# Performance work log

Hardware: AMD Instinct MI355X
Metric: run time of the kernel (lower is better)

The kernel has to match this reference:

```python
import jax, jax.numpy as jnp
import numpy as np

V, E, H, NL, B, T = 32000, 256, 256, 2, 32, 256


def setup_inputs() -> dict:
    key = jax.random.key(0)
    ks = jax.random.split(key, 20)
    s = 0.05
    d = {}
    d['x'] = jax.random.randint(ks[0], (B, T), 0, V)
    d['encoder_output'] = jax.random.normal(ks[1], (T + 1, B, 2 * H), jnp.float32)
    d['encoder_final_state'] = jax.random.normal(ks[2], (2 * NL, B, H), jnp.float32)
    d['embedding'] = jax.random.normal(ks[3], (V, E), jnp.float32) * s
    d['enc_proj_w'] = jax.random.normal(ks[4], (H, 2 * H), jnp.float32) * s
    d['enc_proj_b'] = jnp.zeros((H,), jnp.float32)
    d['attn_wq'] = jax.random.normal(ks[5], (H, H), jnp.float32) * s
    d['attn_wk'] = jax.random.normal(ks[6], (H, H), jnp.float32) * s
    d['attn_wv'] = jax.random.normal(ks[7], (H,), jnp.float32) * s
    d['gru_w_ih0'] = jax.random.normal(ks[8], (3 * H, E + H), jnp.float32) * s
    d['gru_w_hh0'] = jax.random.normal(ks[9], (3 * H, H), jnp.float32) * s
    d['gru_b_ih0'] = jnp.zeros((3 * H,), jnp.float32)
    d['gru_b_hh0'] = jnp.zeros((3 * H,), jnp.float32)
    d['gru_w_ih1'] = jax.random.normal(ks[10], (3 * H, H), jnp.float32) * s
    d['gru_w_hh1'] = jax.random.normal(ks[11], (3 * H, H), jnp.float32) * s
    d['gru_b_ih1'] = jnp.zeros((3 * H,), jnp.float32)
    d['gru_b_hh1'] = jnp.zeros((3 * H,), jnp.float32)
    d['dense_w'] = jax.random.normal(ks[12], (V, H), jnp.float32) * s
    d['dense_b'] = jnp.zeros((V,), jnp.float32)
    return d


def _gru_cell(xin, h, w_ih, w_hh, b_ih, b_hh):
    gi = xin @ w_ih.T + b_ih
    gh = h @ w_hh.T + b_hh
    i_r, i_z, i_n = jnp.split(gi, 3, axis=-1)
    h_r, h_z, h_n = jnp.split(gh, 3, axis=-1)
    r = jax.nn.sigmoid(i_r + h_r)
    z = jax.nn.sigmoid(i_z + h_z)
    n = jnp.tanh(i_n + r * h_n)
    return (1.0 - z) * n + z * h


def _forward(x, encoder_output, encoder_final_state, embedding, enc_proj_w, enc_proj_b,
             attn_wq, attn_wk, attn_wv,
             gru_w_ih0, gru_w_hh0, gru_b_ih0, gru_b_hh0,
             gru_w_ih1, gru_w_hh1, gru_b_ih1, gru_b_hh1,
             dense_w, dense_b):
    Bb, Tt = x.shape
    Hh = enc_proj_w.shape[0]
    L = 2 * Tt  # fixed KV buffer length (= max attention width)
    # project encoder output: (B, T+1, H)
    proj = jnp.einsum('sbd,hd->bsh', encoder_output, enc_proj_w) + enc_proj_b
    # sum forward/backward encoder final states -> (n_layers, B, H)
    h0 = encoder_final_state.reshape(NL, 2, Bb, Hh).sum(axis=1)
    emb = embedding[x].transpose(1, 0, 2)  # (T, B, E)
    # fixed-size KV buffer; slots [0, T+1) hold projected encoder output
    kv0 = jnp.zeros((Bb, L, Hh), proj.dtype).at[:, :Tt + 1, :].set(proj)
    kproj0 = jnp.einsum('blh,gh->blg', kv0, attn_wk)  # precomputed key projections

    def step(carry, inp):
        h, kv, kproj = carry
        emb_t, t = inp
        q = h[-1] @ attn_wq.T  # (B, H)
        scores = jnp.tanh(kproj + q[:, None, :]) @ attn_wv  # (B, L)
        valid = jnp.arange(L) < (Tt + 1 + t)
        attn = jax.nn.softmax(jnp.where(valid[None, :], scores, -1e9), axis=-1)
        attn = attn * valid[None, :].astype(attn.dtype)  # exact zeros at padding
        context = jnp.einsum('bl,blh->bh', attn, kv)
        xin = jnp.concatenate([context, emb_t], axis=-1)  # (B, H+E)
        h0n = _gru_cell(xin, h[0], gru_w_ih0, gru_w_hh0, gru_b_ih0, gru_b_hh0)
        h1n = _gru_cell(h0n, h[1], gru_w_ih1, gru_w_hh1, gru_b_ih1, gru_b_hh1)
        h_new = jnp.stack([h0n, h1n], axis=0)
        out = h1n  # top-layer output for this timestep
        pos = Tt + 1 + t
        kv = jax.lax.dynamic_update_slice_in_dim(kv, out[:, None, :], pos, axis=1)
        kproj = jax.lax.dynamic_update_slice_in_dim(kproj, (out @ attn_wk.T)[:, None, :], pos, axis=1)
        return (h_new, kv, kproj), (out, attn)

    (_, _, _), (outs, attns) = jax.lax.scan(step, (h0, kv0, kproj0), (emb, jnp.arange(Tt)))
    outs = outs.transpose(1, 0, 2)  # (B, T, H)
    logits = jnp.einsum('bth,vh->btv', outs, dense_w) + dense_b  # (B, T, V)
    attn_scores = attns.transpose(1, 0, 2)  # (B, T, 2T)
    return logits, attn_scores


def reference(x, encoder_output, encoder_final_state, embedding, enc_proj_w, enc_proj_b,
              attn_wq, attn_wk, attn_wv,
              gru_w_ih0, gru_w_hh0, gru_b_ih0, gru_b_hh0,
              gru_w_ih1, gru_w_hh1, gru_b_ih1, gru_b_hh1,
              dense_w, dense_b):
    return _forward(x, encoder_output, encoder_final_state, embedding, enc_proj_w, enc_proj_b,
                    attn_wq, attn_wk, attn_wv,
                    gru_w_ih0, gru_w_hh0, gru_b_ih0, gru_b_hh0,
                    gru_w_ih1, gru_w_hh1, gru_b_ih1, gru_b_hh1,
                    dense_w, dense_b)
```

## Files before the change

kernel.cpp:

```cpp
#include <hip/hip_runtime.h>
#include <hip/hip_bf16.h>
#include <hip/hip_fp16.h>

#define NB 32
#define NT 256
#define NH 256
#define NV 32000
#define NL2 512
#define NTP1 257
#define KPS 260

typedef unsigned int u32x4 __attribute__((ext_vector_type(4)));
typedef unsigned int u32x2 __attribute__((ext_vector_type(2)));
typedef short s16x8 __attribute__((ext_vector_type(8)));
typedef float f32x4 __attribute__((ext_vector_type(4)));
typedef float f32x2 __attribute__((ext_vector_type(2)));
typedef _Float16 half2v __attribute__((ext_vector_type(2)));

#define AGENT __HIP_MEMORY_SCOPE_AGENT
__device__ __forceinline__ float aload(const float* p) {
  return __hip_atomic_load((float*)p, __ATOMIC_RELAXED, AGENT);
}
__device__ __forceinline__ void astore(float* p, float v) {
  __hip_atomic_store(p, v, __ATOMIC_RELAXED, AGENT);
}
__device__ __forceinline__ unsigned int aloadu(const unsigned int* p) {
  return __hip_atomic_load((unsigned int*)p, __ATOMIC_RELAXED, AGENT);
}
__device__ __forceinline__ void astoreu(unsigned int* p, unsigned int v) {
  __hip_atomic_store(p, v, __ATOMIC_RELAXED, AGENT);
}

__device__ __forceinline__ float dot2f(half2v a, half2v b, float c) {
#if __has_builtin(__builtin_amdgcn_fdot2)
  return __builtin_amdgcn_fdot2(a, b, c, false);
#else
  return c + (float)a[0] * (float)b[0] + (float)a[1] * (float)b[1];
#endif
}
__device__ __forceinline__ half2v h2(unsigned int u) { return __builtin_bit_cast(half2v, u); }

__device__ __forceinline__ float dotf16(const _Float16* __restrict__ w,
                                        const _Float16* __restrict__ x, int n, float acc) {
#pragma unroll 8
  for (int k = 0; k < n; k += 16) {
    u32x4 a0 = *(const u32x4*)(w + k);
    u32x4 a1 = *(const u32x4*)(w + k + 8);
    u32x4 b0 = *(const u32x4*)(x + k);
    u32x4 b1 = *(const u32x4*)(x + k + 8);
    acc = dot2f(h2(a0.x), h2(b0.x), acc);
    acc = dot2f(h2(a0.y), h2(b0.y), acc);
    acc = dot2f(h2(a0.z), h2(b0.z), acc);
    acc = dot2f(h2(a0.w), h2(b0.w), acc);
    acc = dot2f(h2(a1.x), h2(b1.x), acc);
    acc = dot2f(h2(a1.y), h2(b1.y), acc);
    acc = dot2f(h2(a1.z), h2(b1.z), acc);
    acc = dot2f(h2(a1.w), h2(b1.w), acc);
  }
  return acc;
}

__device__ __forceinline__ float dot16h(const _Float16* __restrict__ w,
                                        const _Float16* __restrict__ x) {
  u32x4 a0 = *(const u32x4*)w;
  u32x4 a1 = *(const u32x4*)(w + 8);
  u32x4 b0 = *(const u32x4*)x;
  u32x4 b1 = *(const u32x4*)(x + 8);
  float acc = 0.f;
  acc = dot2f(h2(a0.x), h2(b0.x), acc);
  acc = dot2f(h2(a0.y), h2(b0.y), acc);
  acc = dot2f(h2(a0.z), h2(b0.z), acc);
  acc = dot2f(h2(a0.w), h2(b0.w), acc);
  acc = dot2f(h2(a1.x), h2(b1.x), acc);
  acc = dot2f(h2(a1.y), h2(b1.y), acc);
  acc = dot2f(h2(a1.z), h2(b1.z), acc);
  acc = dot2f(h2(a1.w), h2(b1.w), acc);
  return acc;
}

__device__ __forceinline__ float fast_tanh(float x) {
  x = fminf(15.f, fmaxf(-15.f, x));
  float e = __expf(2.f * x);
  return 1.f - __fdividef(2.f, e + 1.f);
}
__device__ __forceinline__ float fast_sigmoid(float x) {
  x = fminf(30.f, fmaxf(-30.f, x));
  float e = __expf(-x);
  return __fdividef(1.f, 1.f + e);
}
__device__ __forceinline__ unsigned short f2bf(float f) {
  unsigned int u = __builtin_bit_cast(unsigned int, f);
  return (unsigned short)((u + 0x7FFFu + ((u >> 16) & 1u)) >> 16);
}

__device__ __forceinline__ void batch_barrier(int* __restrict__ ctr, int target) {
  __syncthreads();
  if (threadIdx.x == 0) {
    __hip_atomic_fetch_add(ctr, 1, __ATOMIC_RELEASE, AGENT);
    while (__hip_atomic_load(ctr, __ATOMIC_RELAXED, AGENT) < target)
      __builtin_amdgcn_s_sleep(1);
    asm volatile("" ::: "memory");
  }
  __syncthreads();
}


__global__ void conv_f16_kernel(const float* __restrict__ s, _Float16* __restrict__ d, int n) {
  int i = blockIdx.x * 256 + threadIdx.x;
  if (i < n) d[i] = (_Float16)s[i];
}

__global__ void conv_bf16_kernel(const float* __restrict__ s, unsigned short* __restrict__ d, int n) {
  int i = blockIdx.x * 256 + threadIdx.x;
  if (i < n) d[i] = f2bf(s[i]);
}

__global__ void transpose_kernel(const float* __restrict__ w, float* __restrict__ wT) {
  int i = blockIdx.x * 256 + threadIdx.x;
  if (i < 256 * 512) { int h = i >> 9, dd = i & 511; wT[dd * 256 + h] = w[i]; }
}

__global__ __launch_bounds__(256) void proj_kernel(const float* __restrict__ enc,
                                                   const float* __restrict__ wT,
                                                   const float* __restrict__ pb,
                                                   _Float16* __restrict__ kvT) {
  int gid = blockIdx.x * 256 + threadIdx.x;
  int h4 = gid & 63;
  int bs = gid >> 6;
  if (bs >= NTP1 * NB) return;
  int s = bs >> 5, b = bs & 31;
  const float* er = enc + (size_t)bs * 512;
  float a0 = 0.f, a1 = 0.f, a2 = 0.f, a3 = 0.f;
  for (int d = 0; d < 512; d += 4) {
    f32x4 e4 = *(const f32x4*)(er + d);
    f32x4 w0 = *(const f32x4*)(wT + (size_t)(d + 0) * 256 + h4 * 4);
    f32x4 w1 = *(const f32x4*)(wT + (size_t)(d + 1) * 256 + h4 * 4);
    f32x4 w2 = *(const f32x4*)(wT + (size_t)(d + 2) * 256 + h4 * 4);
    f32x4 w3 = *(const f32x4*)(wT + (size_t)(d + 3) * 256 + h4 * 4);
    a0 = fmaf(e4.x, w0.x, a0); a1 = fmaf(e4.x, w0.y, a1); a2 = fmaf(e4.x, w0.z, a2); a3 = fmaf(e4.x, w0.w, a3);
    a0 = fmaf(e4.y, w1.x, a0); a1 = fmaf(e4.y, w1.y, a1); a2 = fmaf(e4.y, w1.z, a2); a3 = fmaf(e4.y, w1.w, a3);
    a0 = fmaf(e4.z, w2.x, a0); a1 = fmaf(e4.z, w2.y, a1); a2 = fmaf(e4.z, w2.z, a2); a3 = fmaf(e4.z, w2.w, a3);
    a0 = fmaf(e4.w, w3.x, a0); a1 = fmaf(e4.w, w3.y, a1); a2 = fmaf(e4.w, w3.z, a2); a3 = fmaf(e4.w, w3.w, a3);
  }
  int h = h4 * 4;
  a0 += pb[h + 0]; a1 += pb[h + 1]; a2 += pb[h + 2]; a3 += pb[h + 3];
  size_t base = ((size_t)b * NH) * NL2 + s;
  kvT[base + (size_t)(h + 0) * NL2] = (_Float16)a0;
  kvT[base + (size_t)(h + 1) * NL2] = (_Float16)a1;
  kvT[base + (size_t)(h + 2) * NL2] = (_Float16)a2;
  kvT[base + (size_t)(h + 3) * NL2] = (_Float16)a3;
}

__global__ __launch_bounds__(256) void kproj0_kernel(const _Float16* __restrict__ kvT,
                                                     const float* __restrict__ wk,
                                                     _Float16* __restrict__ kprojL) {
  int b = blockIdx.x >> 3, gq = blockIdx.x & 7;
  __shared__ float wks[32][256];
  __shared__ float pk[32][8];
  int tid = threadIdx.x;
  for (int i = tid; i < 32 * 256; i += 256) {
    int g = i >> 8, h = i & 255;
    wks[g][h] = wk[(size_t)(gq * 32 + g) * 256 + h];
  }
  __syncthreads();
  {
    int l = tid;
    float acc[32];
#pragma unroll
    for (int g = 0; g < 32; ++g) acc[g] = 0.f;
    for (int h = 0; h < 256; ++h) {
      float kvv = (float)kvT[((size_t)(b * NH + h)) * NL2 + l];
#pragma unroll
      for (int g = 0; g < 32; ++g) acc[g] = fmaf(kvv, wks[g][h], acc[g]);
    }
    for (int g = 0; g < 32; ++g)
      kprojL[((size_t)b * NL2 + l) * NH + gq * 32 + g] = (_Float16)acc[g];
  }
  {
    int g = tid >> 3, hc = tid & 7;
    float acc = 0.f;
    for (int h = hc * 32; h < hc * 32 + 32; ++h)
      acc += (float)kvT[((size_t)(b * NH + h)) * NL2 + 256] * wks[g][h];
    pk[g][hc] = acc;
    __syncthreads();
    if (tid < 32) {
      float sv = 0.f;
      for (int c = 0; c < 8; ++c) sv += pk[tid][c];
      kprojL[((size_t)b * NL2 + 256) * NH + gq * 32 + tid] = (_Float16)sv;
    }
  }
}


__global__ __launch_bounds__(512) void scan_kernel(
    const int* __restrict__ x, const float* __restrict__ efs, const float* __restrict__ emb,
    const float* __restrict__ wv,
    const float* __restrict__ bih0, const float* __restrict__ bhh0,
    const float* __restrict__ bih1, const float* __restrict__ bhh1,
    const _Float16* __restrict__ wq16, const _Float16* __restrict__ wk16,
    const _Float16* __restrict__ wih0_16, const _Float16* __restrict__ whh0_16,
    const _Float16* __restrict__ wih1_16, const _Float16* __restrict__ whh1_16,
    _Float16* __restrict__ kvT, const _Float16* __restrict__ kprojL,
    float* __restrict__ q_g, float* __restrict__ scores_g, float* __restrict__ xin_gf,
    float* __restrict__ g0i_g, float* __restrict__ g0h_g,
    float* __restrict__ g1i_g, float* __restrict__ g1h_g,
    unsigned int* __restrict__ kstage,
    int* __restrict__ bars,
    unsigned short* __restrict__ outs_bf, float* __restrict__ attn_out) {
  __shared__ __align__(16) float h0s[256], h1s[256], qf[256], wvs[256];
  __shared__ __align__(16) float attnsP[16 * 34], red[16], scratch[544];
  __shared__ __align__(16) _Float16 h0h[256], h1h[256], xinh[512];
  __shared__ __align__(8) _Float16 kp_lds[64 * KPS];

  int tid = threadIdx.x;
  int b = blockIdx.x & 31;
  int s = blockIdx.x >> 5;
  int* bar = bars + b * 32;

  if (tid < 256) {
    float h0v = efs[(size_t)(0 * NB + b) * NH + tid] + efs[(size_t)(1 * NB + b) * NH + tid];
    float h1v = efs[(size_t)(2 * NB + b) * NH + tid] + efs[(size_t)(3 * NB + b) * NH + tid];
    h0s[tid] = h0v; h0h[tid] = (_Float16)h0v;
    h1s[tid] = h1v; h1h[tid] = (_Float16)h1v;
    wvs[tid] = wv[tid];
  }
  {
    int lr = tid >> 3, ch = tid & 7;
    const _Float16* src = kprojL + ((size_t)b * NL2 + 64 * s + lr) * NH + ch * 32;
    _Float16* dst = kp_lds + lr * KPS + ch * 32;
#pragma unroll
    for (int k = 0; k < 32; k += 4)
      *(u32x2*)(dst + k) = *(const u32x2*)(src + k);
  }
  __syncthreads();

  for (int t = 0; t < NT; ++t) {
    int Lt = NTP1 + t;
    int tgt = 8 * (t + 1);
    {
      int row = tid & 31, ch = tid >> 5;
      float p = dot16h(wq16 + (size_t)(32 * s + row) * 256 + ch * 16, h1h + ch * 16);
      scratch[ch * 33 + row] = p;
      if (tid < 32) {
        int tok = x[b * NT + t];
        astore(xin_gf + b * 512 + 256 + 32 * s + tid, emb[(size_t)tok * 256 + 32 * s + tid]);
      }
    }
    __syncthreads();
    if (tid < 32) {
      float a = 0.f;
#pragma unroll
      for (int c = 0; c < 16; ++c) a += scratch[c * 33 + tid];
      astore(q_g + b * 256 + 32 * s + tid, a);
    }
    batch_barrier(bar + 0, tgt);
    if (t > 0 && s == ((Lt - 1) >> 6)) {
      if (tid < 128) {
        unsigned int v = aloadu(kstage + b * 128 + tid);
        *(unsigned int*)(kp_lds + (Lt - 1 - 64 * s) * KPS + 2 * tid) = v;
      }
    }
    if (tid < 256) qf[tid] = aload(q_g + b * 256 + tid);
    __syncthreads();
    {
      int w = tid >> 6, lp = tid & 63;
      int l = 64 * s + lp;
      float part = 0.f;
      if (l < Lt) {
        const _Float16* kp = kp_lds + lp * KPS + 32 * w;
        const float* qh = qf + 32 * w;
        const float* wh = wvs + 32 * w;
#pragma unroll
        for (int j = 0; j < 32; j += 4) {
          u32x2 k4 = *(const u32x2*)(kp + j);
          half2v pa = h2(k4.x), pb = h2(k4.y);
          part = fmaf(wh[j + 0], fast_tanh((float)pa[0] + qh[j + 0]), part);
          part = fmaf(wh[j + 1], fast_tanh((float)pa[1] + qh[j + 1]), part);
          part = fmaf(wh[j + 2], fast_tanh((float)pb[0] + qh[j + 2]), part);
          part = fmaf(wh[j + 3], fast_tanh((float)pb[1] + qh[j + 3]), part);
        }
      }
      scratch[w * 66 + lp] = part;
    }
    __syncthreads();
    if (tid < 64 && 64 * s + tid < Lt) {
      float a = 0.f;
#pragma unroll
      for (int w = 0; w < 8; ++w) a += scratch[w * 66 + tid];
      astore(scores_g + b * 512 + 64 * s + tid, a);
    }
    batch_barrier(bar + 1, tgt);
    {
      float v = (tid < Lt) ? aload(scores_g + b * 512 + tid) : -3.0e38f;
      float m = v;
#pragma unroll
      for (int off = 32; off; off >>= 1) m = fmaxf(m, __shfl_xor(m, off, 64));
      if ((tid & 63) == 0) red[tid >> 6] = m;
      __syncthreads();
      float M = red[0];
#pragma unroll
      for (int i = 1; i < 8; ++i) M = fmaxf(M, red[i]);
      float e = (tid < Lt) ? __expf(v - M) : 0.f;
      float zz = e;
#pragma unroll
      for (int off = 32; off; off >>= 1) zz += __shfl_xor(zz, off, 64);
      if ((tid & 63) == 0) red[8 + (tid >> 6)] = zz;
      __syncthreads();
      float Z = red[8];
#pragma unroll
      for (int i = 1; i < 8; ++i) Z += red[8 + i];
      float a = __fdividef(e, Z);
      attnsP[(tid >> 5) * 34 + (tid & 31)] = a;
      if ((tid >> 6) == s) attn_out[((size_t)(b * NT + t)) * NL2 + tid] = a;
    }
    __syncthreads();
    {
      int h = 32 * s + (tid >> 4), sub = tid & 15;
      const _Float16* kvr = kvT + ((size_t)(b * NH + h)) * NL2 + sub * 32;
      const float* ar = attnsP + sub * 34;
      float a = 0.f;
#pragma unroll
      for (int k = 0; k < 32; k += 8) {
        u32x4 v8 = *(const u32x4*)(kvr + k);
        half2v c0 = h2(v8.x), c1 = h2(v8.y), c2 = h2(v8.z), c3 = h2(v8.w);
        f32x2 a0 = *(const f32x2*)(ar + k);
        f32x2 a1 = *(const f32x2*)(ar + k + 2);
        f32x2 a2 = *(const f32x2*)(ar + k + 4);
        f32x2 a3 = *(const f32x2*)(ar + k + 6);
        a = fmaf((float)c0[0], a0.x, a); a = fmaf((float)c0[1], a0.y, a);
        a = fmaf((float)c1[0], a1.x, a); a = fmaf((float)c1[1], a1.y, a);
        a = fmaf((float)c2[0], a2.x, a); a = fmaf((float)c2[1], a2.y, a);
        a = fmaf((float)c3[0], a3.x, a); a = fmaf((float)c3[1], a3.y, a);
      }
      a += __shfl_xor(a, 1); a += __shfl_xor(a, 2);
      a += __shfl_xor(a, 4); a += __shfl_xor(a, 8);
      if (sub == 0) astore(xin_gf + b * 512 + h, a);
    }
    batch_barrier(bar + 2, tgt);
    if (tid < 512) xinh[tid] = (_Float16)aload(xin_gf + b * 512 + tid);
    __syncthreads();
    if (tid < 384) {
      int r = 96 * s + (tid >> 2), sub = tid & 3;
      float a = dotf16(wih0_16 + (size_t)r * 512 + sub * 128, xinh + sub * 128, 128, 0.f);
      a += __shfl_xor(a, 1); a += __shfl_xor(a, 2);
      if (sub == 0) astore(g0i_g + b * 768 + r, a + bih0[r]);
    } else if (tid < 480) {
      int r = 96 * s + (tid - 384);
      astore(g0h_g + b * 768 + r, dotf16(whh0_16 + (size_t)r * 256, h0h, 256, bhh0[r]));
    }
    batch_barrier(bar + 3, tgt);
    if (tid < 256) {
      float ir = aload(g0i_g + b * 768 + tid),       hr = aload(g0h_g + b * 768 + tid);
      float iz = aload(g0i_g + b * 768 + 256 + tid), hz = aload(g0h_g + b * 768 + 256 + tid);
      float in_ = aload(g0i_g + b * 768 + 512 + tid), hn_ = aload(g0h_g + b * 768 + 512 + tid);
      float r_ = fast_sigmoid(ir + hr);
      float z_ = fast_sigmoid(iz + hz);
      float n_ = fast_tanh(in_ + r_ * hn_);
      float hv = (1.f - z_) * n_ + z_ * h0s[tid];
      h0s[tid] = hv; h0h[tid] = (_Float16)hv;
    }
    __syncthreads();
    if (tid < 384) {
      int r = 96 * s + (tid >> 2), sub = tid & 3;
      float a = dotf16(wih1_16 + (size_t)r * 256 + sub * 64, h0h + sub * 64, 64, 0.f);
      a += __shfl_xor(a, 1); a += __shfl_xor(a, 2);
      if (sub == 0) astore(g1i_g + b * 768 + r, a + bih1[r]);
    } else if (tid < 480) {
      int r = 96 * s + (tid - 384);
      astore(g1h_g + b * 768 + r, dotf16(whh1_16 + (size_t)r * 256, h1h, 256, bhh1[r]));
    }
    batch_barrier(bar + 4, tgt);
    if (tid < 256) {
      float ir = aload(g1i_g + b * 768 + tid),       hr = aload(g1h_g + b * 768 + tid);
      float iz = aload(g1i_g + b * 768 + 256 + tid), hz = aload(g1h_g + b * 768 + 256 + tid);
      float in_ = aload(g1i_g + b * 768 + 512 + tid), hn_ = aload(g1h_g + b * 768 + 512 + tid);
      float r_ = fast_sigmoid(ir + hr);
      float z_ = fast_sigmoid(iz + hz);
      float n_ = fast_tanh(in_ + r_ * hn_);
      float hv = (1.f - z_) * n_ + z_ * h1s[tid];
      h1s[tid] = hv; h1h[tid] = (_Float16)hv;
      if ((tid >> 5) == s) {
        outs_bf[((size_t)(b * NT + t)) * NH + tid] = f2bf(hv);
        if (t < NT - 1) kvT[((size_t)(b * NH + tid)) * NL2 + NTP1 + t] = (_Float16)hv;
      }
    }
    __syncthreads();
    if (t < NT - 1) {
      int row = tid & 31, ch = tid >> 5;
      float p = dot16h(wk16 + (size_t)(32 * s + row) * 256 + ch * 16, h1h + ch * 16);
      scratch[ch * 33 + row] = p;
      __syncthreads();
      if (tid < 32) {
        float a = 0.f;
#pragma unroll
        for (int c = 0; c < 16; ++c) a += scratch[c * 33 + tid];
        unsigned short lo = __builtin_bit_cast(unsigned short, (_Float16)a);
        float an = __shfl_down(a, 1);
        unsigned short hi = __builtin_bit_cast(unsigned short, (_Float16)an);
        if ((tid & 1) == 0)
          astoreu(kstage + b * 128 + 16 * s + (tid >> 1),
                  (unsigned int)lo | ((unsigned int)hi << 16));
      }
      __syncthreads();
    }
  }
}


__global__ __launch_bounds__(256) void logits_gemm(const unsigned short* __restrict__ A,
                                                   const unsigned short* __restrict__ Bw,
                                                   const float* __restrict__ bias,
                                                   float* __restrict__ C) {
  __shared__ unsigned short As[128][88];
  __shared__ unsigned short Bs[128][88];
  int tid = threadIdx.x;
  int nt = blockIdx.x % 250, mt = blockIdx.x / 250;
  int m0 = mt * 128, n0 = nt * 128;
  int lane = tid & 63, w = tid >> 6;
  int wm = w & 1, wn = w >> 1;
  f32x4 acc[4][4];
#pragma unroll
  for (int m = 0; m < 4; ++m)
#pragma unroll
    for (int n = 0; n < 4; ++n) acc[m][n] = (f32x4)0.0f;

  int r0 = tid >> 3;
  int c0 = (tid & 7) * 8;
  for (int kt = 0; kt < 4; ++kt) {
    __syncthreads();
#pragma unroll
    for (int it = 0; it < 4; ++it) {
      int row = it * 32 + r0;
      u32x4 va = *(const u32x4*)(A + (size_t)(m0 + row) * 256 + kt * 64 + c0);
      u32x4 vb = *(const u32x4*)(Bw + (size_t)(n0 + row) * 256 + kt * 64 + c0);
      *(u32x4*)(&As[row][c0]) = va;
      *(u32x4*)(&Bs[row][c0]) = vb;
    }
    __syncthreads();
#pragma unroll
    for (int ks = 0; ks < 2; ++ks) {
      s16x8 af[4], bf[4];
#pragma unroll
      for (int m = 0; m < 4; ++m)
        af[m] = *(const s16x8*)(&As[wm * 64 + m * 16 + (lane & 15)][ks * 32 + (lane >> 4) * 8]);
#pragma unroll
      for (int n = 0; n < 4; ++n)
        bf[n] = *(const s16x8*)(&Bs[wn * 64 + n * 16 + (lane & 15)][ks * 32 + (lane >> 4) * 8]);
#pragma unroll
      for (int m = 0; m < 4; ++m)
#pragma unroll
        for (int n = 0; n < 4; ++n)
          acc[m][n] = __builtin_amdgcn_mfma_f32_16x16x32_bf16(af[m], bf[n], acc[m][n], 0, 0, 0);
    }
  }
#pragma unroll
  for (int n = 0; n < 4; ++n) {
    int col = n0 + wn * 64 + n * 16 + (lane & 15);
    float bv = bias[col];
#pragma unroll
    for (int m = 0; m < 4; ++m) {
      int rowb = m0 + wm * 64 + m * 16 + (lane >> 4) * 4;
#pragma unroll
      for (int r = 0; r < 4; ++r)
        C[(size_t)(rowb + r) * NV + col] = acc[m][n][r] + bv;
    }
  }
}


extern "C" void kernel_launch(void* const* d_in, const int* in_sizes, int n_in,
                              void* d_out, int out_size, void* d_ws, size_t ws_size,
                              hipStream_t stream) {
  const int*   x    = (const int*)d_in[0];
  const float* enc  = (const float*)d_in[1];
  const float* efs  = (const float*)d_in[2];
  const float* emb  = (const float*)d_in[3];
  const float* epw  = (const float*)d_in[4];
  const float* epb  = (const float*)d_in[5];
  const float* wq   = (const float*)d_in[6];
  const float* wk   = (const float*)d_in[7];
  const float* wv   = (const float*)d_in[8];
  const float* wih0 = (const float*)d_in[9];
  const float* whh0 = (const float*)d_in[10];
  const float* bih0 = (const float*)d_in[11];
  const float* bhh0 = (const float*)d_in[12];
  const float* wih1 = (const float*)d_in[13];
  const float* whh1 = (const float*)d_in[14];
  const float* bih1 = (const float*)d_in[15];
  const float* bhh1 = (const float*)d_in[16];
  const float* dw   = (const float*)d_in[17];
  const float* db   = (const float*)d_in[18];

  const size_t o_dwbf   = 0;
  const size_t o_wT     = o_dwbf + 16384000;
  const size_t o_kvT    = o_wT + 524288;
  const size_t o_kproj  = o_kvT + 8388608;
  const size_t o_outs   = o_kproj + 8388608;
  const size_t o_qg     = o_outs + 4194304;
  const size_t o_scores = o_qg + 32768;
  const size_t o_xinf   = o_scores + 65536;
  const size_t o_g0i    = o_xinf + 65536;
  const size_t o_g0h    = o_g0i + 98304;
  const size_t o_g1i    = o_g0h + 98304;
  const size_t o_g1h    = o_g1i + 98304;
  const size_t o_kst    = o_g1h + 98304;
  const size_t o_bar    = o_kst + 16384;
  const size_t need     = o_bar + 4096;
  if (ws_size < need) return;

  char* ws = (char*)d_ws;
  unsigned short* dwbf16 = (unsigned short*)(ws + o_dwbf);
  _Float16* wq16    = (_Float16*)(ws + o_dwbf);
  _Float16* wk16    = (_Float16*)(ws + o_dwbf + 131072);
  _Float16* wih0_16 = (_Float16*)(ws + o_dwbf + 262144);
  _Float16* whh0_16 = (_Float16*)(ws + o_dwbf + 1048576);
  _Float16* wih1_16 = (_Float16*)(ws + o_dwbf + 1441792);
  _Float16* whh1_16 = (_Float16*)(ws + o_dwbf + 1835008);
  float* wT          = (float*)(ws + o_wT);
  _Float16* kvT      = (_Float16*)(ws + o_kvT);
  _Float16* kprojL   = (_Float16*)(ws + o_kproj);
  unsigned short* outs_bf = (unsigned short*)(ws + o_outs);
  float* q_g         = (float*)(ws + o_qg);
  float* scores_g    = (float*)(ws + o_scores);
  float* xin_gf      = (float*)(ws + o_xinf);
  float* g0i_g       = (float*)(ws + o_g0i);
  float* g0h_g       = (float*)(ws + o_g0h);
  float* g1i_g       = (float*)(ws + o_g1i);
  float* g1h_g       = (float*)(ws + o_g1h);
  unsigned int* kstage = (unsigned int*)(ws + o_kst);
  int* bars          = (int*)(ws + o_bar);

  float* logits = (float*)d_out;
  float* attn_out = logits + (size_t)NB * NT * NV;

  hipMemsetAsync(ws + o_kvT, 0, 2 * 8388608, stream);
  hipMemsetAsync(ws + o_bar, 0, 4096, stream);

  conv_f16_kernel<<<(65536 + 255) / 256, 256, 0, stream>>>(wq, wq16, 65536);
  conv_f16_kernel<<<(65536 + 255) / 256, 256, 0, stream>>>(wk, wk16, 65536);
  conv_f16_kernel<<<(393216 + 255) / 256, 256, 0, stream>>>(wih0, wih0_16, 393216);
  conv_f16_kernel<<<(196608 + 255) / 256, 256, 0, stream>>>(whh0, whh0_16, 196608);
  conv_f16_kernel<<<(196608 + 255) / 256, 256, 0, stream>>>(wih1, wih1_16, 196608);
  conv_f16_kernel<<<(196608 + 255) / 256, 256, 0, stream>>>(whh1, whh1_16, 196608);
  transpose_kernel<<<(131072 + 255) / 256, 256, 0, stream>>>(epw, wT);

  proj_kernel<<<(NTP1 * NB * 64) / 256, 256, 0, stream>>>(enc, wT, epb, kvT);
  kproj0_kernel<<<NB * 8, 256, 0, stream>>>(kvT, wk, kprojL);

  scan_kernel<<<256, 512, 0, stream>>>(x, efs, emb, wv, bih0, bhh0, bih1, bhh1,
                                       wq16, wk16, wih0_16, whh0_16, wih1_16, whh1_16,
                                       kvT, kprojL,
                                       q_g, scores_g, xin_gf,
                                       g0i_g, g0h_g, g1i_g, g1h_g, kstage, bars,
                                       outs_bf, attn_out);

  conv_bf16_kernel<<<(8192000 + 255) / 256, 256, 0, stream>>>(dw, dwbf16, 8192000);

  logits_gemm<<<(NB * NT / 128) * (NV / 128), 256, 0, stream>>>(outs_bf, dwbf16, db, logits);
}
```

Measured before the change: 8.125 ms.

## Split scan work by hidden-dim slices with LDS-resident KV and fewer barriers

Restructures the persistent scan kernel so each of the 8 blocks per batch owns a 32-wide hidden slice. That block keeps its slice of both the K-projection and the KV cache in LDS, and computes partial attention scores and partial GRU gate sums over its K-slice. GRU weights are repacked transposed into half2 pairs so that threads read them coalesced. Partial results are reduced through global buffers, which cuts the per-step grid barriers from five to three, removes the kstage exchange, and drops the memset of the KV buffers. The cost is redundant reductions across the 8 partials in every block and more LDS use per block.

```diff
diff --git a/kernel.cpp b/kernel.cpp
--- a/kernel.cpp
+++ b/kernel.cpp
@@ -8,13 +8,11 @@
 #define NV 32000
 #define NL2 512
 #define NTP1 257
-#define KPS 260
 
 typedef unsigned int u32x4 __attribute__((ext_vector_type(4)));
 typedef unsigned int u32x2 __attribute__((ext_vector_type(2)));
 typedef short s16x8 __attribute__((ext_vector_type(8)));
 typedef float f32x4 __attribute__((ext_vector_type(4)));
-typedef float f32x2 __attribute__((ext_vector_type(2)));
 typedef _Float16 half2v __attribute__((ext_vector_type(2)));
 
 #define AGENT __HIP_MEMORY_SCOPE_AGENT
@@ -22,12 +20,6 @@
   return __hip_atomic_load((float*)p, __ATOMIC_RELAXED, AGENT);
 }
 __device__ __forceinline__ void astore(float* p, float v) {
-  __hip_atomic_store(p, v, __ATOMIC_RELAXED, AGENT);
-}
-__device__ __forceinline__ unsigned int aloadu(const unsigned int* p) {
-  return __hip_atomic_load((unsigned int*)p, __ATOMIC_RELAXED, AGENT);
-}
-__device__ __forceinline__ void astoreu(unsigned int* p, unsigned int v) {
   __hip_atomic_store(p, v, __ATOMIC_RELAXED, AGENT);
 }
 
@@ -39,26 +31,6 @@
 #endif
 }
 __device__ __forceinline__ half2v h2(unsigned int u) { return __builtin_bit_cast(half2v, u); }
-
-__device__ __forceinline__ float dotf16(const _Float16* __restrict__ w,
-                                        const _Float16* __restrict__ x, int n, float acc) {
-#pragma unroll 8
-  for (int k = 0; k < n; k += 16) {
-    u32x4 a0 = *(const u32x4*)(w + k);
-    u32x4 a1 = *(const u32x4*)(w + k + 8);
-    u32x4 b0 = *(const u32x4*)(x + k);
-    u32x4 b1 = *(const u32x4*)(x + k + 8);
-    acc = dot2f(h2(a0.x), h2(b0.x), acc);
-    acc = dot2f(h2(a0.y), h2(b0.y), acc);
-    acc = dot2f(h2(a0.z), h2(b0.z), acc);
-    acc = dot2f(h2(a0.w), h2(b0.w), acc);
-    acc = dot2f(h2(a1.x), h2(b1.x), acc);
-    acc = dot2f(h2(a1.y), h2(b1.y), acc);
-    acc = dot2f(h2(a1.z), h2(b1.z), acc);
-    acc = dot2f(h2(a1.w), h2(b1.w), acc);
-  }
-  return acc;
-}
 
 __device__ __forceinline__ float dot16h(const _Float16* __restrict__ w,
                                         const _Float16* __restrict__ x) {
@@ -115,6 +87,17 @@
   if (i < n) d[i] = f2bf(s[i]);
 }
 
+__global__ void packT_kernel(const float* __restrict__ w, unsigned int* __restrict__ out,
+                             int R, int K) {
+  int gid = blockIdx.x * 256 + threadIdx.x;
+  int K2 = K >> 1;
+  if (gid >= R * K2) return;
+  int k2 = gid / R, r = gid - k2 * R;
+  unsigned short ua = __builtin_bit_cast(unsigned short, (_Float16)w[(size_t)r * K + 2 * k2]);
+  unsigned short ub = __builtin_bit_cast(unsigned short, (_Float16)w[(size_t)r * K + 2 * k2 + 1]);
+  out[(size_t)k2 * R + r] = (unsigned int)ua | ((unsigned int)ub << 16);
+}
+
 __global__ void transpose_kernel(const float* __restrict__ w, float* __restrict__ wT) {
   int i = blockIdx.x * 256 + threadIdx.x;
   if (i < 256 * 512) { int h = i >> 9, dd = i & 511; wT[dd * 256 + h] = w[i]; }
@@ -123,7 +106,7 @@
 __global__ __launch_bounds__(256) void proj_kernel(const float* __restrict__ enc,
                                                    const float* __restrict__ wT,
                                                    const float* __restrict__ pb,
-                                                   _Float16* __restrict__ kvT) {
+                                                   _Float16* __restrict__ kvL) {
   int gid = blockIdx.x * 256 + threadIdx.x;
   int h4 = gid & 63;
   int bs = gid >> 6;
@@ -144,14 +127,12 @@
   }
   int h = h4 * 4;
   a0 += pb[h + 0]; a1 += pb[h + 1]; a2 += pb[h + 2]; a3 += pb[h + 3];
-  size_t base = ((size_t)b * NH) * NL2 + s;
-  kvT[base + (size_t)(h + 0) * NL2] = (_Float16)a0;
-  kvT[base + (size_t)(h + 1) * NL2] = (_Float16)a1;
-  kvT[base + (size_t)(h + 2) * NL2] = (_Float16)a2;
-  kvT[base + (size_t)(h + 3) * NL2] = (_Float16)a3;
-}
-
-__global__ __launch_bounds__(256) void kproj0_kernel(const _Float16* __restrict__ kvT,
+  _Float16* dst = kvL + ((size_t)b * 512 + s) * 256 + h;
+  dst[0] = (_Float16)a0; dst[1] = (_Float16)a1;
+  dst[2] = (_Float16)a2; dst[3] = (_Float16)a3;
+}
+
+__global__ __launch_bounds__(256) void kproj0_kernel(const _Float16* __restrict__ kvL,
                                                      const float* __restrict__ wk,
                                                      _Float16* __restrict__ kprojL) {
   int b = blockIdx.x >> 3, gq = blockIdx.x & 7;
@@ -169,7 +150,7 @@
 #pragma unroll
     for (int g = 0; g < 32; ++g) acc[g] = 0.f;
     for (int h = 0; h < 256; ++h) {
-      float kvv = (float)kvT[((size_t)(b * NH + h)) * NL2 + l];
+      float kvv = (float)kvL[((size_t)b * 512 + l) * 256 + h];
 #pragma unroll
       for (int g = 0; g < 32; ++g) acc[g] = fmaf(kvv, wks[g][h], acc[g]);
     }
@@ -180,7 +161,7 @@
     int g = tid >> 3, hc = tid & 7;
     float acc = 0.f;
     for (int h = hc * 32; h < hc * 32 + 32; ++h)
-      acc += (float)kvT[((size_t)(b * NH + h)) * NL2 + 256] * wks[g][h];
+      acc += (float)kvL[((size_t)b * 512 + 256) * 256 + h] * wks[g][h];
     pk[g][hc] = acc;
     __syncthreads();
     if (tid < 32) {
@@ -198,19 +179,19 @@
     const float* __restrict__ bih0, const float* __restrict__ bhh0,
     const float* __restrict__ bih1, const float* __restrict__ bhh1,
     const _Float16* __restrict__ wq16, const _Float16* __restrict__ wk16,
-    const _Float16* __restrict__ wih0_16, const _Float16* __restrict__ whh0_16,
-    const _Float16* __restrict__ wih1_16, const _Float16* __restrict__ whh1_16,
-    _Float16* __restrict__ kvT, const _Float16* __restrict__ kprojL,
-    float* __restrict__ q_g, float* __restrict__ scores_g, float* __restrict__ xin_gf,
-    float* __restrict__ g0i_g, float* __restrict__ g0h_g,
-    float* __restrict__ g1i_g, float* __restrict__ g1h_g,
-    unsigned int* __restrict__ kstage,
+    const unsigned int* __restrict__ wih0T, const unsigned int* __restrict__ whh0T,
+    const unsigned int* __restrict__ wih1T, const unsigned int* __restrict__ whh1T,
+    const unsigned int* __restrict__ kvL_u, const unsigned int* __restrict__ kprojL_u,
+    float* __restrict__ spart, float* __restrict__ vec0, float* __restrict__ vec1,
     int* __restrict__ bars,
     unsigned short* __restrict__ outs_bf, float* __restrict__ attn_out) {
-  __shared__ __align__(16) float h0s[256], h1s[256], qf[256], wvs[256];
-  __shared__ __align__(16) float attnsP[16 * 34], red[16], scratch[544];
-  __shared__ __align__(16) _Float16 h0h[256], h1h[256], xinh[512];
-  __shared__ __align__(8) _Float16 kp_lds[64 * KPS];
+  __shared__ __align__(16) unsigned int kp_u[512 * 17];
+  __shared__ __align__(16) unsigned int kv_u[512 * 19];
+  __shared__ __align__(16) float att[512], gsum[1024];
+  __shared__ __align__(16) float h0s[256], h1s[256];
+  __shared__ __align__(16) float scr[544], scr2[32 * 35];
+  __shared__ __align__(16) float qs[32], wvs[32], red[16];
+  __shared__ __align__(16) _Float16 h0h[256], h1h[256], xinh[64];
 
   int tid = threadIdx.x;
   int b = blockIdx.x & 31;
@@ -222,15 +203,17 @@
     float h1v = efs[(size_t)(2 * NB + b) * NH + tid] + efs[(size_t)(3 * NB + b) * NH + tid];
     h0s[tid] = h0v; h0h[tid] = (_Float16)h0v;
     h1s[tid] = h1v; h1h[tid] = (_Float16)h1v;
-    wvs[tid] = wv[tid];
-  }
-  {
-    int lr = tid >> 3, ch = tid & 7;
-    const _Float16* src = kprojL + ((size_t)b * NL2 + 64 * s + lr) * NH + ch * 32;
-    _Float16* dst = kp_lds + lr * KPS + ch * 32;
-#pragma unroll
-    for (int k = 0; k < 32; k += 4)
-      *(u32x2*)(dst + k) = *(const u32x2*)(src + k);
+  }
+  if (tid < 32) wvs[tid] = wv[32 * s + tid];
+  for (int idx = tid; idx < 257 * 16; idx += 512) {
+    int l = idx >> 4, c = idx & 15;
+    kp_u[l * 17 + c] = kprojL_u[((size_t)b * 512 + l) * 128 + 16 * s + c];
+    kv_u[l * 19 + c] = kvL_u[((size_t)b * 512 + l) * 128 + 16 * s + c];
+  }
+  for (int idx = tid; idx < 255 * 16; idx += 512) {
+    int l = 257 + (idx >> 4), c = idx & 15;
+    kp_u[l * 17 + c] = 0u;
+    kv_u[l * 19 + c] = 0u;
   }
   __syncthreads();
 
@@ -239,59 +222,40 @@
     int tgt = 8 * (t + 1);
     {
       int row = tid & 31, ch = tid >> 5;
-      float p = dot16h(wq16 + (size_t)(32 * s + row) * 256 + ch * 16, h1h + ch * 16);
-      scratch[ch * 33 + row] = p;
-      if (tid < 32) {
+      scr[ch * 33 + row] = dot16h(wq16 + (size_t)(32 * s + row) * 256 + ch * 16, h1h + ch * 16);
+      if (tid >= 480) {
+        int j = tid - 480;
         int tok = x[b * NT + t];
-        astore(xin_gf + b * 512 + 256 + 32 * s + tid, emb[(size_t)tok * 256 + 32 * s + tid]);
+        xinh[32 + j] = (_Float16)emb[(size_t)tok * 256 + 32 * s + j];
       }
     }
     __syncthreads();
     if (tid < 32) {
       float a = 0.f;
 #pragma unroll
-      for (int c = 0; c < 16; ++c) a += scratch[c * 33 + tid];
-      astore(q_g + b * 256 + 32 * s + tid, a);
+      for (int c = 0; c < 16; ++c) a += scr[c * 33 + tid];
+      qs[tid] = a;
+    }
+    __syncthreads();
+    {
+      float acc = 0.f;
+      if (tid < Lt) {
+        const unsigned int* kr = kp_u + tid * 17;
+#pragma unroll 4
+        for (int g2 = 0; g2 < 16; ++g2) {
+          half2v kp2 = h2(kr[g2]);
+          acc = fmaf(wvs[2 * g2 + 0], fast_tanh((float)kp2[0] + qs[2 * g2 + 0]), acc);
+          acc = fmaf(wvs[2 * g2 + 1], fast_tanh((float)kp2[1] + qs[2 * g2 + 1]), acc);
+        }
+      }
+      astore(spart + ((size_t)(b * 8 + s)) * 512 + tid, acc);
     }
     batch_barrier(bar + 0, tgt);
-    if (t > 0 && s == ((Lt - 1) >> 6)) {
-      if (tid < 128) {
-        unsigned int v = aloadu(kstage + b * 128 + tid);
-        *(unsigned int*)(kp_lds + (Lt - 1 - 64 * s) * KPS + 2 * tid) = v;
-      }
-    }
-    if (tid < 256) qf[tid] = aload(q_g + b * 256 + tid);
-    __syncthreads();
-    {
-      int w = tid >> 6, lp = tid & 63;
-      int l = 64 * s + lp;
-      float part = 0.f;
-      if (l < Lt) {
-        const _Float16* kp = kp_lds + lp * KPS + 32 * w;
-        const float* qh = qf + 32 * w;
-        const float* wh = wvs + 32 * w;
-#pragma unroll
-        for (int j = 0; j < 32; j += 4) {
-          u32x2 k4 = *(const u32x2*)(kp + j);
-          half2v pa = h2(k4.x), pb = h2(k4.y);
-          part = fmaf(wh[j + 0], fast_tanh((float)pa[0] + qh[j + 0]), part);
-          part = fmaf(wh[j + 1], fast_tanh((float)pa[1] + qh[j + 1]), part);
-          part = fmaf(wh[j + 2], fast_tanh((float)pb[0] + qh[j + 2]), part);
-          part = fmaf(wh[j + 3], fast_tanh((float)pb[1] + qh[j + 3]), part);
-        }
-      }
-      scratch[w * 66 + lp] = part;
-    }
-    __syncthreads();
-    if (tid < 64 && 64 * s + tid < Lt) {
-      float a = 0.f;
-#pragma unroll
-      for (int w = 0; w < 8; ++w) a += scratch[w * 66 + tid];
-      astore(scores_g + b * 512 + 64 * s + tid, a);
-    }
-    batch_barrier(bar + 1, tgt);
-    {
-      float v = (tid < Lt) ? aload(scores_g + b * 512 + tid) : -3.0e38f;
+    {
+      float sum = 0.f;
+#pragma unroll
+      for (int sp = 0; sp < 8; ++sp) sum += aload(spart + ((size_t)(b * 8 + sp)) * 512 + tid);
+      float v = (tid < Lt) ? sum : -3.0e38f;
       float m = v;
 #pragma unroll
       for (int off = 32; off; off >>= 1) m = fmaxf(m, __shfl_xor(m, off, 64));
@@ -310,96 +274,140 @@
 #pragma unroll
       for (int i = 1; i < 8; ++i) Z += red[8 + i];
       float a = __fdividef(e, Z);
-      attnsP[(tid >> 5) * 34 + (tid & 31)] = a;
+      att[tid] = a;
       if ((tid >> 6) == s) attn_out[((size_t)(b * NT + t)) * NL2 + tid] = a;
     }
     __syncthreads();
     {
-      int h = 32 * s + (tid >> 4), sub = tid & 15;
-      const _Float16* kvr = kvT + ((size_t)(b * NH + h)) * NL2 + sub * 32;
-      const float* ar = attnsP + sub * 34;
+      int c = tid >> 4, hh = tid & 15;
+      float aA = 0.f, aB = 0.f;
+#pragma unroll
+      for (int j = 0; j < 16; ++j) {
+        int l = 16 * c + j;
+        half2v kv2 = h2(kv_u[l * 19 + hh]);
+        float av = att[l];
+        aA = fmaf((float)kv2[0], av, aA);
+        aB = fmaf((float)kv2[1], av, aB);
+      }
+      scr2[c * 35 + 2 * hh] = aA;
+      scr2[c * 35 + 2 * hh + 1] = aB;
+    }
+    __syncthreads();
+    if (tid < 32) {
       float a = 0.f;
 #pragma unroll
-      for (int k = 0; k < 32; k += 8) {
-        u32x4 v8 = *(const u32x4*)(kvr + k);
-        half2v c0 = h2(v8.x), c1 = h2(v8.y), c2 = h2(v8.z), c3 = h2(v8.w);
-        f32x2 a0 = *(const f32x2*)(ar + k);
-        f32x2 a1 = *(const f32x2*)(ar + k + 2);
-        f32x2 a2 = *(const f32x2*)(ar + k + 4);
-        f32x2 a3 = *(const f32x2*)(ar + k + 6);
-        a = fmaf((float)c0[0], a0.x, a); a = fmaf((float)c0[1], a0.y, a);
-        a = fmaf((float)c1[0], a1.x, a); a = fmaf((float)c1[1], a1.y, a);
-        a = fmaf((float)c2[0], a2.x, a); a = fmaf((float)c2[1], a2.y, a);
-        a = fmaf((float)c3[0], a3.x, a); a = fmaf((float)c3[1], a3.y, a);
-      }
-      a += __shfl_xor(a, 1); a += __shfl_xor(a, 2);
-      a += __shfl_xor(a, 4); a += __shfl_xor(a, 8);
-      if (sub == 0) astore(xin_gf + b * 512 + h, a);
+      for (int c = 0; c < 32; ++c) a += scr2[c * 35 + tid];
+      xinh[tid] = (_Float16)a;
+    }
+    __syncthreads();
+    {
+      const unsigned int* xu = (const unsigned int*)xinh;
+      const unsigned int* h0u = (const unsigned int*)h0h;
+      float accA = 0.f, accI = 0.f, accH = 0.f;
+      bool dual = (tid < 256);
+#pragma unroll 2
+      for (int i = 0; i < 16; ++i) {
+        unsigned int xc = xu[i], xe = xu[16 + i];
+        const unsigned int* wc = wih0T + (size_t)(16 * s + i) * 768;
+        const unsigned int* we = wih0T + (size_t)(128 + 16 * s + i) * 768;
+        accA = dot2f(h2(wc[tid]), h2(xc), accA);
+        accA = dot2f(h2(we[tid]), h2(xe), accA);
+        if (dual) {
+          accI = dot2f(h2(wc[512 + tid]), h2(xc), accI);
+          accI = dot2f(h2(we[512 + tid]), h2(xe), accI);
+        }
+      }
+#pragma unroll 2
+      for (int i = 0; i < 16; ++i) {
+        unsigned int hv = h0u[16 * s + i];
+        const unsigned int* wr = whh0T + (size_t)(16 * s + i) * 768;
+        accA = dot2f(h2(wr[tid]), h2(hv), accA);
+        if (dual) accH = dot2f(h2(wr[512 + tid]), h2(hv), accH);
+      }
+      float* vb = vec0 + (size_t)(b * 8 + s) * 1024;
+      astore(vb + tid, accA);
+      if (dual) { astore(vb + 512 + tid, accI); astore(vb + 768 + tid, accH); }
+    }
+    batch_barrier(bar + 1, tgt);
+    {
+      float t0 = 0.f, t1 = 0.f;
+#pragma unroll
+      for (int sp = 0; sp < 8; ++sp) {
+        const float* vb = vec0 + (size_t)(b * 8 + sp) * 1024;
+        t0 += aload(vb + tid);
+        t1 += aload(vb + 512 + tid);
+      }
+      gsum[tid] = t0; gsum[512 + tid] = t1;
+    }
+    __syncthreads();
+    if (tid < 256) {
+      float rr = fast_sigmoid(gsum[tid] + bih0[tid] + bhh0[tid]);
+      float zz = fast_sigmoid(gsum[256 + tid] + bih0[256 + tid] + bhh0[256 + tid]);
+      float nn = fast_tanh(gsum[512 + tid] + bih0[512 + tid] + rr * (gsum[768 + tid] + bhh0[512 + tid]));
+      float hv = (1.f - zz) * nn + zz * h0s[tid];
+      h0s[tid] = hv; h0h[tid] = (_Float16)hv;
+    }
+    __syncthreads();
+    {
+      const unsigned int* h0u = (const unsigned int*)h0h;
+      const unsigned int* h1u = (const unsigned int*)h1h;
+      float accA = 0.f, accI = 0.f, accH = 0.f;
+      bool dual = (tid < 256);
+#pragma unroll 2
+      for (int i = 0; i < 16; ++i) {
+        unsigned int xv = h0u[16 * s + i];
+        unsigned int hv = h1u[16 * s + i];
+        const unsigned int* wi = wih1T + (size_t)(16 * s + i) * 768;
+        const unsigned int* wh = whh1T + (size_t)(16 * s + i) * 768;
+        accA = dot2f(h2(wi[tid]), h2(xv), accA);
+        accA = dot2f(h2(wh[tid]), h2(hv), accA);
+        if (dual) {
+          accI = dot2f(h2(wi[512 + tid]), h2(xv), accI);
+          accH = dot2f(h2(wh[512 + tid]), h2(hv), accH);
+        }
+      }
+      float* vb = vec1 + (size_t)(b * 8 + s) * 1024;
+      astore(vb + tid, accA);
+      if (dual) { astore(vb + 512 + tid, accI); astore(vb + 768 + tid, accH); }
     }
     batch_barrier(bar + 2, tgt);
-    if (tid < 512) xinh[tid] = (_Float16)aload(xin_gf + b * 512 + tid);
-    __syncthreads();
-    if (tid < 384) {
-      int r = 96 * s + (tid >> 2), sub = tid & 3;
-      float a = dotf16(wih0_16 + (size_t)r * 512 + sub * 128, xinh + sub * 128, 128, 0.f);
-      a += __shfl_xor(a, 1); a += __shfl_xor(a, 2);
-      if (sub == 0) astore(g0i_g + b * 768 + r, a + bih0[r]);
-    } else if (tid < 480) {
-      int r = 96 * s + (tid - 384);
-      astore(g0h_g + b * 768 + r, dotf16(whh0_16 + (size_t)r * 256, h0h, 256, bhh0[r]));
-    }
-    batch_barrier(bar + 3, tgt);
+    {
+      float t0 = 0.f, t1 = 0.f;
+#pragma unroll
+      for (int sp = 0; sp < 8; ++sp) {
+        const float* vb = vec1 + (size_t)(b * 8 + sp) * 1024;
+        t0 += aload(vb + tid);
+        t1 += aload(vb + 512 + tid);
+      }
+      gsum[tid] = t0; gsum[512 + tid] = t1;
+    }
+    __syncthreads();
     if (tid < 256) {
-      float ir = aload(g0i_g + b * 768 + tid),       hr = aload(g0h_g + b * 768 + tid);
-      float iz = aload(g0i_g + b * 768 + 256 + tid), hz = aload(g0h_g + b * 768 + 256 + tid);
-      float in_ = aload(g0i_g + b * 768 + 512 + tid), hn_ = aload(g0h_g + b * 768 + 512 + tid);
-      float r_ = fast_sigmoid(ir + hr);
-      float z_ = fast_sigmoid(iz + hz);
-      float n_ = fast_tanh(in_ + r_ * hn_);
-      float hv = (1.f - z_) * n_ + z_ * h0s[tid];
-      h0s[tid] = hv; h0h[tid] = (_Float16)hv;
-    }
-    __syncthreads();
-    if (tid < 384) {
-      int r = 96 * s + (tid >> 2), sub = tid & 3;
-      float a = dotf16(wih1_16 + (size_t)r * 256 + sub * 64, h0h + sub * 64, 64, 0.f);
-      a += __shfl_xor(a, 1); a += __shfl_xor(a, 2);
-      if (sub == 0) astore(g1i_g + b * 768 + r, a + bih1[r]);
-    } else if (tid < 480) {
-      int r = 96 * s + (tid - 384);
-      astore(g1h_g + b * 768 + r, dotf16(whh1_16 + (size_t)r * 256, h1h, 256, bhh1[r]));
-    }
-    batch_barrier(bar + 4, tgt);
-    if (tid < 256) {
-      float ir = aload(g1i_g + b * 768 + tid),       hr = aload(g1h_g + b * 768 + tid);
-      float iz = aload(g1i_g + b * 768 + 256 + tid), hz = aload(g1h_g + b * 768 + 256 + tid);
-      float in_ = aload(g1i_g + b * 768 + 512 + tid), hn_ = aload(g1h_g + b * 768 + 512 + tid);
-      float r_ = fast_sigmoid(ir + hr);
-      float z_ = fast_sigmoid(iz + hz);
-      float n_ = fast_tanh(in_ + r_ * hn_);
-      float hv = (1.f - z_) * n_ + z_ * h1s[tid];
+      float rr = fast_sigmoid(gsum[tid] + bih1[tid] + bhh1[tid]);
+      float zz = fast_sigmoid(gsum[256 + tid] + bih1[256 + tid] + bhh1[256 + tid]);
+      float nn = fast_tanh(gsum[512 + tid] + bih1[512 + tid] + rr * (gsum[768 + tid] + bhh1[512 + tid]));
+      float hv = (1.f - zz) * nn + zz * h1s[tid];
       h1s[tid] = hv; h1h[tid] = (_Float16)hv;
-      if ((tid >> 5) == s) {
-        outs_bf[((size_t)(b * NT + t)) * NH + tid] = f2bf(hv);
-        if (t < NT - 1) kvT[((size_t)(b * NH + tid)) * NL2 + NTP1 + t] = (_Float16)hv;
-      }
+      if ((tid >> 5) == s) outs_bf[((size_t)(b * NT + t)) * NH + tid] = f2bf(hv);
     }
     __syncthreads();
     if (t < NT - 1) {
-      int row = tid & 31, ch = tid >> 5;
-      float p = dot16h(wk16 + (size_t)(32 * s + row) * 256 + ch * 16, h1h + ch * 16);
-      scratch[ch * 33 + row] = p;
+      int pos = NTP1 + t;
+      if (tid < 16) {
+        unsigned short lo = __builtin_bit_cast(unsigned short, h1h[32 * s + 2 * tid]);
+        unsigned short hi = __builtin_bit_cast(unsigned short, h1h[32 * s + 2 * tid + 1]);
+        kv_u[pos * 19 + tid] = (unsigned int)lo | ((unsigned int)hi << 16);
+      }
+      {
+        int row = tid & 31, ch = tid >> 5;
+        scr[ch * 33 + row] = dot16h(wk16 + (size_t)(32 * s + row) * 256 + ch * 16, h1h + ch * 16);
+      }
       __syncthreads();
       if (tid < 32) {
         float a = 0.f;
 #pragma unroll
-        for (int c = 0; c < 16; ++c) a += scratch[c * 33 + tid];
-        unsigned short lo = __builtin_bit_cast(unsigned short, (_Float16)a);
-        float an = __shfl_down(a, 1);
-        unsigned short hi = __builtin_bit_cast(unsigned short, (_Float16)an);
-        if ((tid & 1) == 0)
-          astoreu(kstage + b * 128 + 16 * s + (tid >> 1),
-                  (unsigned int)lo | ((unsigned int)hi << 16));
+        for (int c = 0; c < 16; ++c) a += scr[c * 33 + tid];
+        ((_Float16*)kp_u)[pos * 34 + tid] = (_Float16)a;
       }
       __syncthreads();
     }
@@ -491,67 +499,61 @@
   const float* dw   = (const float*)d_in[17];
   const float* db   = (const float*)d_in[18];
 
-  const size_t o_dwbf   = 0;
-  const size_t o_wT     = o_dwbf + 16384000;
-  const size_t o_kvT    = o_wT + 524288;
-  const size_t o_kproj  = o_kvT + 8388608;
-  const size_t o_outs   = o_kproj + 8388608;
-  const size_t o_qg     = o_outs + 4194304;
-  const size_t o_scores = o_qg + 32768;
-  const size_t o_xinf   = o_scores + 65536;
-  const size_t o_g0i    = o_xinf + 65536;
-  const size_t o_g0h    = o_g0i + 98304;
-  const size_t o_g1i    = o_g0h + 98304;
-  const size_t o_g1h    = o_g1i + 98304;
-  const size_t o_kst    = o_g1h + 98304;
-  const size_t o_bar    = o_kst + 16384;
+  const size_t o_alias  = 0;
+  const size_t a_wq16   = 0;
+  const size_t a_wk16   = a_wq16 + 131072;
+  const size_t a_wih0T  = a_wk16 + 131072;
+  const size_t a_whh0T  = a_wih0T + 786432;
+  const size_t a_wih1T  = a_whh0T + 393216;
+  const size_t a_whh1T  = a_wih1T + 393216;
+  const size_t a_kvL    = a_whh1T + 393216;
+  const size_t o_wT     = o_alias + 16384000;
+  const size_t o_kprojL = o_wT + 524288;
+  const size_t o_outs   = o_kprojL + 8388608;
+  const size_t o_spart  = o_outs + 4194304;
+  const size_t o_vec0   = o_spart + 524288;
+  const size_t o_vec1   = o_vec0 + 1048576;
+  const size_t o_bar    = o_vec1 + 1048576;
   const size_t need     = o_bar + 4096;
   if (ws_size < need) return;
 
   char* ws = (char*)d_ws;
-  unsigned short* dwbf16 = (unsigned short*)(ws + o_dwbf);
-  _Float16* wq16    = (_Float16*)(ws + o_dwbf);
-  _Float16* wk16    = (_Float16*)(ws + o_dwbf + 131072);
-  _Float16* wih0_16 = (_Float16*)(ws + o_dwbf + 262144);
-  _Float16* whh0_16 = (_Float16*)(ws + o_dwbf + 1048576);
-  _Float16* wih1_16 = (_Float16*)(ws + o_dwbf + 1441792);
-  _Float16* whh1_16 = (_Float16*)(ws + o_dwbf + 1835008);
+  unsigned short* dwbf16 = (unsigned short*)(ws + o_alias);
+  _Float16* wq16     = (_Float16*)(ws + a_wq16);
+  _Float16* wk16     = (_Float16*)(ws + a_wk16);
+  unsigned int* wih0T = (unsigned int*)(ws + a_wih0T);
+  unsigned int* whh0T = (unsigned int*)(ws + a_whh0T);
+  unsigned int* wih1T = (unsigned int*)(ws + a_wih1T);
+  unsigned int* whh1T = (unsigned int*)(ws + a_whh1T);
+  _Float16* kvL      = (_Float16*)(ws + a_kvL);
   float* wT          = (float*)(ws + o_wT);
-  _Float16* kvT      = (_Float16*)(ws + o_kvT);
-  _Float16* kprojL   = (_Float16*)(ws + o_kproj);
+  _Float16* kprojL   = (_Float16*)(ws + o_kprojL);
   unsigned short* outs_bf = (unsigned short*)(ws + o_outs);
-  float* q_g         = (float*)(ws + o_qg);
-  float* scores_g    = (float*)(ws + o_scores);
-  float* xin_gf      = (float*)(ws + o_xinf);
-  float* g0i_g       = (float*)(ws + o_g0i);
-  float* g0h_g       = (float*)(ws + o_g0h);
-  float* g1i_g       = (float*)(ws + o_g1i);
-  float* g1h_g       = (float*)(ws + o_g1h);
-  unsigned int* kstage = (unsigned int*)(ws + o_kst);
+  float* spart       = (float*)(ws + o_spart);
+  float* vec0        = (float*)(ws + o_vec0);
+  float* vec1        = (float*)(ws + o_vec1);
   int* bars          = (int*)(ws + o_bar);
 
   float* logits = (float*)d_out;
   float* attn_out = logits + (size_t)NB * NT * NV;
 
-  hipMemsetAsync(ws + o_kvT, 0, 2 * 8388608, stream);
   hipMemsetAsync(ws + o_bar, 0, 4096, stream);
 
   conv_f16_kernel<<<(65536 + 255) / 256, 256, 0, stream>>>(wq, wq16, 65536);
   conv_f16_kernel<<<(65536 + 255) / 256, 256, 0, stream>>>(wk, wk16, 65536);
-  conv_f16_kernel<<<(393216 + 255) / 256, 256, 0, stream>>>(wih0, wih0_16, 393216);
-  conv_f16_kernel<<<(196608 + 255) / 256, 256, 0, stream>>>(whh0, whh0_16, 196608);
-  conv_f16_kernel<<<(196608 + 255) / 256, 256, 0, stream>>>(wih1, wih1_16, 196608);
-  conv_f16_kernel<<<(196608 + 255) / 256, 256, 0, stream>>>(whh1, whh1_16, 196608);
+  packT_kernel<<<(768 * 256 + 255) / 256, 256, 0, stream>>>(wih0, wih0T, 768, 512);
+  packT_kernel<<<(768 * 128 + 255) / 256, 256, 0, stream>>>(whh0, whh0T, 768, 256);
+  packT_kernel<<<(768 * 128 + 255) / 256, 256, 0, stream>>>(wih1, wih1T, 768, 256);
+  packT_kernel<<<(768 * 128 + 255) / 256, 256, 0, stream>>>(whh1, whh1T, 768, 256);
   transpose_kernel<<<(131072 + 255) / 256, 256, 0, stream>>>(epw, wT);
 
-  proj_kernel<<<(NTP1 * NB * 64) / 256, 256, 0, stream>>>(enc, wT, epb, kvT);
-  kproj0_kernel<<<NB * 8, 256, 0, stream>>>(kvT, wk, kprojL);
+  proj_kernel<<<(NTP1 * NB * 64) / 256, 256, 0, stream>>>(enc, wT, epb, kvL);
+  kproj0_kernel<<<NB * 8, 256, 0, stream>>>(kvL, wk, kprojL);
 
   scan_kernel<<<256, 512, 0, stream>>>(x, efs, emb, wv, bih0, bhh0, bih1, bhh1,
-                                       wq16, wk16, wih0_16, whh0_16, wih1_16, whh1_16,
-                                       kvT, kprojL,
-                                       q_g, scores_g, xin_gf,
-                                       g0i_g, g0h_g, g1i_g, g1h_g, kstage, bars,
+                                       wq16, wk16, wih0T, whh0T, wih1T, whh1T,
+                                       (const unsigned int*)kvL, (const unsigned int*)kprojL,
+                                       spart, vec0, vec1, bars,
                                        outs_bf, attn_out);
 
   conv_bf16_kernel<<<(8192000 + 255) / 256, 256, 0, stream>>>(dw, dwbf16, 8192000);
```

New measurement: 7.129 ms. -12.3%, faster.
